# Kernel optimization log

Measured on AMD Instinct MI355X. Metric: run time of the kernel, lower is better.

## Reference

```python
import jax, jax.numpy as jnp
import numpy as np

NP, NR, NK = 64, 8, 500          # problems, rollouts, candidate nodes
H, HEADS, VD = 256, 8, 8         # hidden_dim, heads, vars_dim
HD = H // HEADS                  # head_dim
CLIP = 10.0                      # tanh logit clipping
NEG_INF = -jnp.inf


def setup_inputs() -> dict:
    key = jax.random.key(0)
    ks = jax.random.split(key, 17)
    f = lambda k, s: jax.random.normal(k, s, dtype=jnp.float32)
    B = NP * NR
    s = 1.0 / np.sqrt(H)
    return {
        "X": f(ks[0], (NP, NK, H)),
        "K": f(ks[1], (HEADS, NP, NK, HD)),
        "V": f(ks[2], (HEADS, NP, NK, HD)),
        "query": f(ks[3], (B, H)),
        "state1": f(ks[4], (B, H)),
        "state2": f(ks[5], (B, H)),
        "varfeat": f(ks[6], (NP, VD, NK)),
        "mask": jax.random.uniform(ks[7], (NP, NR, NK)) < 0.1,
        "nn_Q": f(ks[8], (HEADS, H, HD)) * (1.0 / np.sqrt(HD)),
        "nn_O": f(ks[9], (H, H)) * s,
        "nn_A": f(ks[10], (VD, H)) * s,
        "nn_B": f(ks[11], (H,)) * s,
        "nn_W": f(ks[12], (H,)) * s,
        "W_ih": f(ks[13], (4 * H, H)) * s,
        "W_hh": f(ks[14], (4 * H, H)) * s,
        "b_ih": f(ks[15], (4 * H,)) * s,
        "b_hh": f(ks[16], (4 * H,)) * s,
    }


def _decode(X, K, V, query, state1, state2, varfeat, mask,
            nn_Q, nn_O, nn_A, nn_B, nn_W, W_ih, W_hh, b_ih, b_hh):
    B = query.shape[0]
    # --- LSTMCell (PyTorch gate order: i, f, g, o) ---
    gates = query @ W_ih.T + b_ih + state1 @ W_hh.T + b_hh
    i, fg, g, o = jnp.split(gates, 4, axis=1)
    c = jax.nn.sigmoid(fg) * state2 + jax.nn.sigmoid(i) * jnp.tanh(g)
    h = jax.nn.sigmoid(o) * jnp.tanh(c)
    # --- MultiHeadAttention (glimpse) ---
    q = h.reshape(NP, NR, H)
    Q = jnp.einsum('pqh,ahd->apqd', q, nn_Q)                    # [heads,NP,NR,HD]
    S = jnp.einsum('apqd,apkd->apqk', Q, K) * (1.0 / np.sqrt(HD))
    S = jnp.where(mask[None], NEG_INF, S)
    S = jax.nn.softmax(S, axis=-1)
    x = jnp.einsum('apqk,apkd->apqd', S, V)
    x = x.transpose(1, 2, 0, 3).reshape(NP, NR, H)              # [NP,NR,H]
    qm = x @ nn_O                                               # glimpse query
    # --- additive attention with variable features ---
    vf = jnp.einsum('pvk,vh->pkh', varfeat, nn_A) + nn_B        # [NP,NK,H]
    t = jnp.tanh(X[:, None] + vf[:, None] + qm[:, :, None])     # [NP,NR,NK,H]
    logit = jnp.einsum('pqkh,h->pqk', t, nn_W)
    logit = jnp.where(mask, NEG_INF, logit).reshape(B, NK)
    # --- choose (mode=1: greedy argmax) ---
    infeasible = logit == NEG_INF
    l = jnp.where(infeasible, NEG_INF, jnp.tanh(logit) * CLIP)
    chosen = jnp.argmax(l, axis=1)
    logp = jax.nn.log_softmax(l, axis=1)
    chosen_p = jnp.take_along_axis(logp, chosen[:, None], axis=1).squeeze(1)
    return h, c, chosen_p


def reference(X, K, V, query, state1, state2, varfeat, mask,
              nn_Q, nn_O, nn_A, nn_B, nn_W, W_ih, W_hh, b_ih, b_hh):
    return _decode(X, K, V, query, state1, state2, varfeat, mask,
                   nn_Q, nn_O, nn_A, nn_B, nn_W, W_ih, W_hh, b_ih, b_hh)
```

## Files before the change

### kernel.cpp

```cpp
#include <hip/hip_runtime.h>

#define NPP   64
#define NRR   8
#define NKK   500
#define HDIM  256
#define NHEAD 8
#define VDIM  8
#define HD    32
#define BTOT  512

__device__ __forceinline__ float fast_tanh(float x) {
  const float e = __expf(2.f * x);
  return 1.f - 2.f * __builtin_amdgcn_rcpf(e + 1.f);
}
__device__ __forceinline__ float fast_sig(float x) {
  return __builtin_amdgcn_rcpf(1.f + __expf(-x));
}

__global__ __launch_bounds__(64) void k_lstm4(
    const float* __restrict__ query, const float* __restrict__ state1,
    const float* __restrict__ state2,
    const float* __restrict__ W_ih, const float* __restrict__ W_hh,
    const float* __restrict__ b_ih, const float* __restrict__ b_hh,
    const unsigned char* __restrict__ maskb, int* __restrict__ flagp,
    float* __restrict__ out_h, float* __restrict__ out_c)
{
  __shared__ float Wt[32][40];
  __shared__ float At[32][40];
  __shared__ float gt[32][40];

  const int t  = threadIdx.x;
  const int hb = blockIdx.x;
  const int bb = blockIdx.y;

  if (flagp != nullptr && hb == 0 && bb == 0) {
    __shared__ int f;
    if (t == 0) f = 0;
    __syncthreads();
    int any = 0;
    for (int j = t; j < 2048; j += 64) any |= maskb[2 * j + 1];
    if (any) atomicOr(&f, 1);
    __syncthreads();
    if (t == 0) *flagp = f;
  }

  const int tr = t >> 3, tc = t & 7;
  const int srow = t >> 1, sseg = (t & 1) * 16;
  const int wgrow = (srow >> 3) * HDIM + hb * 8 + (srow & 7);
  const int agrow = bb * 32 + srow;

  float acc[4][4];
#pragma unroll
  for (int i = 0; i < 4; ++i)
#pragma unroll
    for (int j = 0; j < 4; ++j) acc[i][j] = 0.f;

  for (int k0 = 0; k0 < 512; k0 += 32) {
    __syncthreads();
    {
      const float* wsrc = (k0 < 256) ? (W_ih + (size_t)wgrow * HDIM + k0)
                                     : (W_hh + (size_t)wgrow * HDIM + (k0 - 256));
      const float* asrc = (k0 < 256) ? (query  + (size_t)agrow * HDIM + k0)
                                     : (state1 + (size_t)agrow * HDIM + (k0 - 256));
#pragma unroll
      for (int j = 0; j < 4; ++j) {
        const float4 wv = *reinterpret_cast<const float4*>(wsrc + sseg + 4 * j);
        const float4 av = *reinterpret_cast<const float4*>(asrc + sseg + 4 * j);
        const int kk = sseg + 4 * j;
        Wt[kk + 0][srow] = wv.x; Wt[kk + 1][srow] = wv.y;
        Wt[kk + 2][srow] = wv.z; Wt[kk + 3][srow] = wv.w;
        At[kk + 0][srow] = av.x; At[kk + 1][srow] = av.y;
        At[kk + 2][srow] = av.z; At[kk + 3][srow] = av.w;
      }
    }
    __syncthreads();
#pragma unroll 8
    for (int kk = 0; kk < 32; ++kk) {
      const float4 wv = *reinterpret_cast<const float4*>(&Wt[kk][tr * 4]);
      const float4 av = *reinterpret_cast<const float4*>(&At[kk][tc * 4]);
      const float w[4] = {wv.x, wv.y, wv.z, wv.w};
      const float a[4] = {av.x, av.y, av.z, av.w};
#pragma unroll
      for (int i = 0; i < 4; ++i)
#pragma unroll
        for (int j = 0; j < 4; ++j) acc[i][j] += w[i] * a[j];
    }
  }

#pragma unroll
  for (int i = 0; i < 4; ++i) {
    float4 v;
    v.x = acc[i][0]; v.y = acc[i][1]; v.z = acc[i][2]; v.w = acc[i][3];
    *reinterpret_cast<float4*>(&gt[tr * 4 + i][tc * 4]) = v;
  }
  __syncthreads();

#pragma unroll
  for (int it = 0; it < 4; ++it) {
    const int cell = t + 64 * it;
    const int b = cell & 31, h = cell >> 5;
    const int gh = hb * 8 + h;
    const int gb = bb * 32 + b;
    const float bi = b_ih[0 * HDIM + gh] + b_hh[0 * HDIM + gh];
    const float bf = b_ih[1 * HDIM + gh] + b_hh[1 * HDIM + gh];
    const float bg = b_ih[2 * HDIM + gh] + b_hh[2 * HDIM + gh];
    const float bo = b_ih[3 * HDIM + gh] + b_hh[3 * HDIM + gh];
    const float iv = fast_sig (gt[ 0 + h][b] + bi);
    const float fv = fast_sig (gt[ 8 + h][b] + bf);
    const float gv = fast_tanh(gt[16 + h][b] + bg);
    const float ov = fast_sig (gt[24 + h][b] + bo);
    const size_t off = (size_t)gb * HDIM + gh;
    const float c = fv * state2[off] + iv * gv;
    out_c[off] = c;
    out_h[off] = ov * fast_tanh(c);
  }
}

__global__ __launch_bounds__(512, 4) void k_attn8(
    const float* __restrict__ Kt, const float* __restrict__ Vt,
    const float* __restrict__ nn_Q, const float* __restrict__ nn_O,
    const void* __restrict__ maskp, const int* __restrict__ flagp,
    const float* __restrict__ out_h, float* __restrict__ qm_slabs)
{
  const int p = blockIdx.x >> 3;
  const int a = blockIdx.x & 7;
  const int t = threadIdx.x;
  const int wave = t >> 6, lane = t & 63;

  __shared__ float hs[NRR][HDIM];
  __shared__ float Qs[NRR][36];
  __shared__ float Sb[NRR][512];
  __shared__ float pb[16][NRR][HD];
  __shared__ float xs[NRR][36];

  const float4 hv = reinterpret_cast<const float4*>(
      out_h + (size_t)p * NRR * HDIM)[t];

  const int flag = *flagp;

  const int kc = (t < NKK) ? t : (NKK - 1);
  const float4* kp4 = reinterpret_cast<const float4*>(
      Kt + (((size_t)a * NPP + p) * NKK + kc) * HD);
  float4 kreg[8];
#pragma unroll
  for (int j = 0; j < 8; ++j) kreg[j] = kp4[j];

  const int dpv = t & 31, kb = t >> 5;
  const float* vb = Vt + (((size_t)a * NPP + p) * NKK + (size_t)kb * 32) * HD + dpv;
  float vreg[32];
#pragma unroll
  for (int j = 0; j < 32; ++j)
    vreg[j] = (kb * 32 + j < NKK) ? vb[(size_t)j * HD] : 0.f;

  float maskv[NRR];
  {
    const unsigned char* mb = (const unsigned char*)maskp;
    const int* mi = (const int*)maskp;
#pragma unroll
    for (int r = 0; r < NRR; ++r) {
      const size_t mo = (size_t)(p * NRR + r) * NKK + kc;
      const bool mk = flag ? (mb[mo] != 0) : (mi[mo] != 0);
      maskv[r] = mk ? -INFINITY : 0.f;
    }
  }

  reinterpret_cast<float4*>(&hs[0][0])[t] = hv;
  __syncthreads();

  {
    const int r = wave, d4 = lane >> 3, ks = lane & 7;
    const float* qb = nn_Q + ((size_t)a * HDIM + ks * 32) * HD + d4 * 4;
    float qx = 0.f, qy = 0.f, qz = 0.f, qw = 0.f;
#pragma unroll
    for (int h = 0; h < 32; ++h) {
      const float hval = hs[r][ks * 32 + h];
      const float4 wv = *reinterpret_cast<const float4*>(qb + (size_t)h * HD);
      qx += hval * wv.x; qy += hval * wv.y;
      qz += hval * wv.z; qw += hval * wv.w;
    }
#pragma unroll
    for (int off = 1; off < 8; off <<= 1) {
      qx += __shfl_xor(qx, off, 64);
      qy += __shfl_xor(qy, off, 64);
      qz += __shfl_xor(qz, off, 64);
      qw += __shfl_xor(qw, off, 64);
    }
    if (ks == 0) {
      const float sc = 0.17677669529663687f;
      Qs[r][d4 * 4 + 0] = qx * sc; Qs[r][d4 * 4 + 1] = qy * sc;
      Qs[r][d4 * 4 + 2] = qz * sc; Qs[r][d4 * 4 + 3] = qw * sc;
    }
  }
  __syncthreads();

#pragma unroll
  for (int r = 0; r < NRR; ++r) {
    float s = 0.f;
#pragma unroll
    for (int j = 0; j < 8; ++j) {
      const float4 q = *reinterpret_cast<const float4*>(&Qs[r][j * 4]);
      const float4 k4 = kreg[j];
      s += q.x * k4.x + q.y * k4.y + q.z * k4.z + q.w * k4.w;
    }
    Sb[r][t] = (t < NKK) ? (s + maskv[r]) : -INFINITY;
  }
  __syncthreads();

  {
    const int r = wave;
    float lv[8], m = -INFINITY;
#pragma unroll
    for (int i = 0; i < 8; ++i) {
      lv[i] = Sb[r][lane + 64 * i];
      m = fmaxf(m, lv[i]);
    }
#pragma unroll
    for (int off = 32; off > 0; off >>= 1) m = fmaxf(m, __shfl_xor(m, off, 64));
    float ssum = 0.f;
#pragma unroll
    for (int i = 0; i < 8; ++i) {
      lv[i] = __expf(lv[i] - m);
      ssum += lv[i];
    }
#pragma unroll
    for (int off = 32; off > 0; off >>= 1) ssum += __shfl_xor(ssum, off, 64);
    const float inv = 1.f / ssum;
#pragma unroll
    for (int i = 0; i < 8; ++i) Sb[r][lane + 64 * i] = lv[i] * inv;
  }
  __syncthreads();

  {
    float acc[NRR];
#pragma unroll
    for (int r = 0; r < NRR; ++r) acc[r] = 0.f;
#pragma unroll
    for (int j4 = 0; j4 < 8; ++j4) {
      const float v0 = vreg[j4 * 4 + 0], v1 = vreg[j4 * 4 + 1];
      const float v2 = vreg[j4 * 4 + 2], v3 = vreg[j4 * 4 + 3];
#pragma unroll
      for (int r = 0; r < NRR; ++r) {
        const float4 s4 = *reinterpret_cast<const float4*>(
            &Sb[r][kb * 32 + j4 * 4]);
        acc[r] += s4.x * v0 + s4.y * v1 + s4.z * v2 + s4.w * v3;
      }
    }
#pragma unroll
    for (int r = 0; r < NRR; ++r) pb[kb][r][dpv] = acc[r];
  }
  __syncthreads();

  if (t < 256) {
    const int r = t >> 5, d = t & 31;
    float s = 0.f;
#pragma unroll
    for (int q = 0; q < 16; ++q) s += pb[q][r][d];
    xs[r][d] = s;
  }
  __syncthreads();

  {
    const int j = t & 255, rr = t >> 8;
    float a0 = 0.f, a1 = 0.f, a2 = 0.f, a3 = 0.f;
#pragma unroll
    for (int d4 = 0; d4 < 8; ++d4) {
      const float4 x0 = *reinterpret_cast<const float4*>(&xs[rr * 4 + 0][d4 * 4]);
      const float4 x1 = *reinterpret_cast<const float4*>(&xs[rr * 4 + 1][d4 * 4]);
      const float4 x2 = *reinterpret_cast<const float4*>(&xs[rr * 4 + 2][d4 * 4]);
      const float4 x3 = *reinterpret_cast<const float4*>(&xs[rr * 4 + 3][d4 * 4]);
      const float c0[4] = {x0.x, x0.y, x0.z, x0.w};
      const float c1[4] = {x1.x, x1.y, x1.z, x1.w};
      const float c2[4] = {x2.x, x2.y, x2.z, x2.w};
      const float c3[4] = {x3.x, x3.y, x3.z, x3.w};
#pragma unroll
      for (int dd = 0; dd < 4; ++dd) {
        const float w = nn_O[((size_t)(a * HD + d4 * 4 + dd)) * HDIM + j];
        a0 += c0[dd] * w; a1 += c1[dd] * w;
        a2 += c2[dd] * w; a3 += c3[dd] * w;
      }
    }
    float* slab = qm_slabs + (size_t)a * BTOT * HDIM;
    slab[(size_t)(p * NRR + rr * 4 + 0) * HDIM + j] = a0;
    slab[(size_t)(p * NRR + rr * 4 + 1) * HDIM + j] = a1;
    slab[(size_t)(p * NRR + rr * 4 + 2) * HDIM + j] = a2;
    slab[(size_t)(p * NRR + rr * 4 + 3) * HDIM + j] = a3;
  }
}

__global__ __launch_bounds__(256) void k_logits6(
    const float* __restrict__ X, const float* __restrict__ varfeat,
    const float* __restrict__ nn_A, const float* __restrict__ nn_B,
    const float* __restrict__ nn_W, const float* __restrict__ qm_slabs,
    const int* __restrict__ flagp, const void* __restrict__ maskp,
    float* __restrict__ pmax, float* __restrict__ psum)
{
  const int p  = blockIdx.x >> 5;
  const int kt = blockIdx.x & 31;
  const int t = threadIdx.x;
  const int wave = t >> 6, lane = t & 63;
  const int h0 = lane * 4;

  __shared__ float qb[NRR][260];
  __shared__ float red[4][NRR][2];

  const unsigned char* mb = (const unsigned char*)maskp;
  const int* mi = (const int*)maskp;
  const int flag = *flagp;
  const bool mbyte = (flag != 0);

  for (int s = t; s < 512; s += 256) {
    const int r = s >> 6, h4 = s & 63;
    const float4 bv = *reinterpret_cast<const float4*>(nn_B + h4 * 4);
    float qx = bv.x, qy = bv.y, qz = bv.z, qw = bv.w;
#pragma unroll
    for (int a = 0; a < NHEAD; ++a) {
      const float4 q = *reinterpret_cast<const float4*>(
          qm_slabs + (size_t)a * BTOT * HDIM +
          (size_t)(p * NRR + r) * HDIM + h4 * 4);
      qx += q.x; qy += q.y; qz += q.z; qw += q.w;
    }
    qb[r][h4 * 4 + 0] = qx; qb[r][h4 * 4 + 1] = qy;
    qb[r][h4 * 4 + 2] = qz; qb[r][h4 * 4 + 3] = qw;
  }
  __syncthreads();

  const float4 w4 = *reinterpret_cast<const float4*>(nn_W + h0);
  float4 a4r[VDIM];
#pragma unroll
  for (int v = 0; v < VDIM; ++v)
    a4r[v] = *reinterpret_cast<const float4*>(nn_A + (size_t)v * HDIM + h0);
  float4 q4r[NRR];
#pragma unroll
  for (int r = 0; r < NRR; ++r)
    q4r[r] = *reinterpret_cast<const float4*>(&qb[r][h0]);

  float rmax = -INFINITY, rsum = 0.f;

  for (int kk = 0; kk < 4; ++kk) {
    const int k = kt * 16 + wave * 4 + kk;
    if (k >= NKK) break;

    const float4 x4 = *reinterpret_cast<const float4*>(
        X + ((size_t)p * NKK + k) * HDIM + h0);
    float base0 = x4.x, base1 = x4.y, base2 = x4.z, base3 = x4.w;
#pragma unroll
    for (int v = 0; v < VDIM; ++v) {
      const float vv = varfeat[((size_t)p * VDIM + v) * NKK + k];
      base0 += vv * a4r[v].x; base1 += vv * a4r[v].y;
      base2 += vv * a4r[v].z; base3 += vv * a4r[v].w;
    }

    float acc[NRR];
#pragma unroll
    for (int r = 0; r < NRR; ++r) {
      acc[r] = fast_tanh(base0 + q4r[r].x) * w4.x
             + fast_tanh(base1 + q4r[r].y) * w4.y
             + fast_tanh(base2 + q4r[r].z) * w4.z
             + fast_tanh(base3 + q4r[r].w) * w4.w;
    }

    float v4[4];
    {
      float sw[8];
#pragma unroll
      for (int j = 0; j < 8; ++j) sw[j] = __shfl_xor(acc[j], 32, 64);
      const bool hi = (lane & 32) != 0;
#pragma unroll
      for (int j = 0; j < 4; ++j)
        v4[j] = hi ? (acc[j + 4] + sw[j + 4]) : (acc[j] + sw[j]);
    }
    float v2[2];
    {
      float sw[4];
#pragma unroll
      for (int j = 0; j < 4; ++j) sw[j] = __shfl_xor(v4[j], 16, 64);
      const bool hi = (lane & 16) != 0;
      v2[0] = hi ? (v4[2] + sw[2]) : (v4[0] + sw[0]);
      v2[1] = hi ? (v4[3] + sw[3]) : (v4[1] + sw[1]);
    }
    float w;
    {
      const float s0 = __shfl_xor(v2[0], 8, 64);
      const float s1 = __shfl_xor(v2[1], 8, 64);
      w = ((lane & 8) != 0) ? (v2[1] + s1) : (v2[0] + s0);
    }
    w += __shfl_xor(w, 4, 64);
    w += __shfl_xor(w, 2, 64);
    w += __shfl_xor(w, 1, 64);

    if ((lane & 7) == 0) {
      const int r = lane >> 3;
      const size_t mrow = (size_t)(p * NRR + r) * NKK + k;
      const bool mk = mbyte ? (mb[mrow] != 0) : (mi[mrow] != 0);
      const float l = mk ? -INFINITY : fast_tanh(w) * 10.0f;
      rmax = fmaxf(rmax, l);
      rsum += __expf(l - 10.f);
    }
  }

  if ((lane & 7) == 0) {
    red[wave][lane >> 3][0] = rmax;
    red[wave][lane >> 3][1] = rsum;
  }
  __syncthreads();
  if (t < NRR) {
    float m = red[0][t][0], s = red[0][t][1];
#pragma unroll
    for (int w = 1; w < 4; ++w) {
      m = fmaxf(m, red[w][t][0]);
      s += red[w][t][1];
    }
    pmax[(size_t)(p * NRR + t) * 32 + kt] = m;
    psum[(size_t)(p * NRR + t) * 32 + kt] = s;
  }
}

__global__ __launch_bounds__(64) void k_choose2(
    const float* __restrict__ pmax, const float* __restrict__ psum,
    float* __restrict__ out_p)
{
  const int b = blockIdx.x;
  const int lane = threadIdx.x;
  float m = (lane < 32) ? pmax[(size_t)b * 32 + lane] : -INFINITY;
  float s = (lane < 32) ? psum[(size_t)b * 32 + lane] : 0.f;
#pragma unroll
  for (int off = 16; off > 0; off >>= 1) {
    m = fmaxf(m, __shfl_xor(m, off, 64));
    s += __shfl_xor(s, off, 64);
  }
  if (lane == 0) out_p[b] = m - 10.f - logf(s);
}

__global__ __launch_bounds__(256) void k_fused(
    const float* __restrict__ X, const float* __restrict__ Kt,
    const float* __restrict__ Vt, const float* __restrict__ varfeat,
    const void* __restrict__ maskp,
    const float* __restrict__ nn_Q, const float* __restrict__ nn_O,
    const float* __restrict__ nn_A, const float* __restrict__ nn_B,
    const float* __restrict__ nn_W,
    const float* __restrict__ out_h, float* __restrict__ out_p)
{
  const int p = blockIdx.x >> 3;
  const int r = blockIdx.x & 7;
  const int t = threadIdx.x;
  const int wave = t >> 6, lane = t & 63;

  __shared__ float hs[HDIM];
  __shared__ float Qs[NHEAD][HD];
  __shared__ float Sb[NHEAD][NKK];
  __shared__ float xs[HDIM];
  __shared__ float qs[HDIM];
  __shared__ float As2[HDIM][VDIM];
  __shared__ float Ws[HDIM];
  __shared__ float lsb[NKK];
  __shared__ int   mask_any;

  const unsigned char* mb = (const unsigned char*)maskp;
  if (t == 0) mask_any = 0;
  __syncthreads();
  {
    int any = 0;
    for (int j = t; j < 2048; j += 256) any |= mb[2 * j + 1];
    if (any) atomicOr(&mask_any, 1);
  }
  for (int idx = t; idx < VDIM * HDIM; idx += 256)
    As2[idx & 255][idx >> 8] = nn_A[idx];
  Ws[t] = nn_W[t];
  hs[t] = out_h[(size_t)(p * NRR + r) * HDIM + t];
  __syncthreads();
  const bool mbyte = (mask_any != 0);
  const int* mi = (const int*)maskp;
  const size_t mrow = (size_t)(p * NRR + r) * NKK;
  {
    const int a = t >> 5, d = t & 31;
    const float* nq = nn_Q + (size_t)a * HDIM * HD + d;
    float acc = 0.f;
    for (int h = 0; h < HDIM; ++h) acc += hs[h] * nq[(size_t)h * HD];
    Qs[a][d] = acc * 0.17677669529663687f;
  }
  __syncthreads();
  for (int k = t; k < NKK; k += 256) {
    const bool mk = mbyte ? (mb[mrow + k] != 0) : (mi[mrow + k] != 0);
#pragma unroll
    for (int a = 0; a < NHEAD; ++a) {
      const float4* kr4 = reinterpret_cast<const float4*>(
          Kt + (((size_t)a * NPP + p) * NKK + k) * HD);
      float s = 0.f;
#pragma unroll
      for (int d4 = 0; d4 < HD / 4; ++d4) {
        const float4 u = kr4[d4];
        s += Qs[a][4 * d4] * u.x + Qs[a][4 * d4 + 1] * u.y
           + Qs[a][4 * d4 + 2] * u.z + Qs[a][4 * d4 + 3] * u.w;
      }
      Sb[a][k] = mk ? -INFINITY : s;
    }
  }
  __syncthreads();
  for (int aa = 0; aa < 2; ++aa) {
    const int a = wave * 2 + aa;
    float m = -INFINITY;
    for (int k = lane; k < NKK; k += 64) m = fmaxf(m, Sb[a][k]);
#pragma unroll
    for (int off = 32; off > 0; off >>= 1) m = fmaxf(m, __shfl_xor(m, off, 64));
    float ssum = 0.f;
    for (int k = lane; k < NKK; k += 64) {
      const float e = expf(Sb[a][k] - m);
      Sb[a][k] = e; ssum += e;
    }
#pragma unroll
    for (int off = 32; off > 0; off >>= 1) ssum += __shfl_xor(ssum, off, 64);
    const float inv = 1.f / ssum;
    for (int k = lane; k < NKK; k += 64) Sb[a][k] *= inv;
  }
  __syncthreads();
  {
    const int a = t >> 5, d = t & 31;
    const float* vb = Vt + ((size_t)a * NPP + p) * NKK * HD + d;
    float acc = 0.f;
    for (int k = 0; k < NKK; ++k) acc += Sb[a][k] * vb[(size_t)k * HD];
    xs[a * HD + d] = acc;
  }
  __syncthreads();
  {
    float acc = 0.f;
    for (int i = 0; i < HDIM; ++i) acc += xs[i] * nn_O[(size_t)i * HDIM + t];
    qs[t] = acc + nn_B[t];
  }
  __syncthreads();
  for (int k = t; k < NKK; k += 256) {
    float vfv[VDIM];
#pragma unroll
    for (int v = 0; v < VDIM; ++v)
      vfv[v] = varfeat[((size_t)p * VDIM + v) * NKK + k];
    const float4* xp4 = reinterpret_cast<const float4*>(
        X + ((size_t)p * NKK + k) * HDIM);
    float acc = 0.f;
    for (int h4 = 0; h4 < HDIM / 4; ++h4) {
      const float4 ux = xp4[h4];
      const float xv[4] = {ux.x, ux.y, ux.z, ux.w};
#pragma unroll
      for (int j = 0; j < 4; ++j) {
        const int h = 4 * h4 + j;
        float base = xv[j] + qs[h];
        const float4 a0 = *reinterpret_cast<const float4*>(&As2[h][0]);
        const float4 a1 = *reinterpret_cast<const float4*>(&As2[h][4]);
        base += vfv[0] * a0.x + vfv[1] * a0.y + vfv[2] * a0.z + vfv[3] * a0.w
              + vfv[4] * a1.x + vfv[5] * a1.y + vfv[6] * a1.z + vfv[7] * a1.w;
        acc += tanhf(base) * Ws[h];
      }
    }
    lsb[k] = acc;
  }
  __syncthreads();
  for (int k = t; k < NKK; k += 256) {
    const bool mk = mbyte ? (mb[mrow + k] != 0) : (mi[mrow + k] != 0);
    lsb[k] = mk ? -INFINITY : tanhf(lsb[k]) * 10.0f;
  }
  __syncthreads();
  if (wave == 0) {
    float m = -INFINITY;
    for (int k = lane; k < NKK; k += 64) m = fmaxf(m, lsb[k]);
#pragma unroll
    for (int off = 32; off > 0; off >>= 1) m = fmaxf(m, __shfl_xor(m, off, 64));
    float s = 0.f;
    for (int k = lane; k < NKK; k += 64) s += expf(lsb[k] - m);
#pragma unroll
    for (int off = 32; off > 0; off >>= 1) s += __shfl_xor(s, off, 64);
    if (lane == 0) out_p[p * NRR + r] = -logf(s);
  }
}

extern "C" void kernel_launch(void* const* d_in, const int* in_sizes, int n_in,
                              void* d_out, int out_size, void* d_ws, size_t ws_size,
                              hipStream_t stream)
{
  const float* X       = (const float*)d_in[0];
  const float* Kt      = (const float*)d_in[1];
  const float* Vt      = (const float*)d_in[2];
  const float* query   = (const float*)d_in[3];
  const float* state1  = (const float*)d_in[4];
  const float* state2  = (const float*)d_in[5];
  const float* varfeat = (const float*)d_in[6];
  const void*  maskp   = d_in[7];
  const float* nn_Q    = (const float*)d_in[8];
  const float* nn_O    = (const float*)d_in[9];
  const float* nn_A    = (const float*)d_in[10];
  const float* nn_B    = (const float*)d_in[11];
  const float* nn_W    = (const float*)d_in[12];
  const float* W_ih    = (const float*)d_in[13];
  const float* W_hh    = (const float*)d_in[14];
  const float* b_ih    = (const float*)d_in[15];
  const float* b_hh    = (const float*)d_in[16];

  float* out   = (float*)d_out;
  float* out_h = out;
  float* out_c = out + (size_t)BTOT * HDIM;
  float* out_p = out + (size_t)2 * BTOT * HDIM;

  const size_t flag_bytes = 256;
  const size_t qm8_bytes  = (size_t)NHEAD * BTOT * HDIM * 4;
  const size_t part_bytes = (size_t)BTOT * 32 * 4;
  const size_t need = flag_bytes + qm8_bytes + 2 * part_bytes;

  if (ws_size >= need) {
    int*   flagp = (int*)d_ws;
    float* qmw  = (float*)((char*)d_ws + flag_bytes);
    float* pmax = (float*)((char*)d_ws + flag_bytes + qm8_bytes);
    float* psum = (float*)((char*)d_ws + flag_bytes + qm8_bytes + part_bytes);

    hipLaunchKernelGGL(k_lstm4, dim3(32, 16), dim3(64), 0, stream,
                       query, state1, state2, W_ih, W_hh, b_ih, b_hh,
                       (const unsigned char*)maskp, flagp, out_h, out_c);
    hipLaunchKernelGGL(k_attn8, dim3(NPP * NHEAD), dim3(512), 0, stream,
                       Kt, Vt, nn_Q, nn_O, maskp, flagp, out_h, qmw);
    hipLaunchKernelGGL(k_logits6, dim3(NPP * 32), dim3(256), 0, stream,
                       X, varfeat, nn_A, nn_B, nn_W, qmw, flagp, maskp,
                       pmax, psum);
    hipLaunchKernelGGL(k_choose2, dim3(BTOT), dim3(64), 0, stream,
                       pmax, psum, out_p);
  } else {
    hipLaunchKernelGGL(k_lstm4, dim3(32, 16), dim3(64), 0, stream,
                       query, state1, state2, W_ih, W_hh, b_ih, b_hh,
                       (const unsigned char*)maskp, nullptr, out_h, out_c);
    hipLaunchKernelGGL(k_fused, dim3(NPP * NRR), dim3(256), 0, stream,
                       X, Kt, Vt, varfeat, maskp,
                       nn_Q, nn_O, nn_A, nn_B, nn_W,
                       out_h, out_p);
  }
}
```

Baseline: 234.9 us.

## Widen LSTM blocks to 256 threads and split attention across rollout halves

The LSTM gate GEMM now runs 256 threads per block, each computing a 2x2 tile instead of 4x4, with padded shared tiles. The attention kernel is launched with twice as many blocks, each handling 4 of the 8 rollouts. The Q projection is split across two wave groups and summed afterwards. This raises parallelism and occupancy for small grids, at the cost of loading the K/V registers twice (once per half) and adding extra syncs.

```diff
diff --git a/kernel.cpp b/kernel.cpp
--- a/kernel.cpp
+++ b/kernel.cpp
@@ -17,7 +17,7 @@
   return __builtin_amdgcn_rcpf(1.f + __expf(-x));
 }
 
-__global__ __launch_bounds__(64) void k_lstm4(
+__global__ __launch_bounds__(256) void k_lstm3(
     const float* __restrict__ query, const float* __restrict__ state1,
     const float* __restrict__ state2,
     const float* __restrict__ W_ih, const float* __restrict__ W_hh,
@@ -25,9 +25,9 @@
     const unsigned char* __restrict__ maskb, int* __restrict__ flagp,
     float* __restrict__ out_h, float* __restrict__ out_c)
 {
-  __shared__ float Wt[32][40];
-  __shared__ float At[32][40];
-  __shared__ float gt[32][40];
+  __shared__ float Wt[32][33];
+  __shared__ float At[32][33];
+  __shared__ float gt[32][33];
 
   const int t  = threadIdx.x;
   const int hb = blockIdx.x;
@@ -38,67 +38,54 @@
     if (t == 0) f = 0;
     __syncthreads();
     int any = 0;
-    for (int j = t; j < 2048; j += 64) any |= maskb[2 * j + 1];
+    for (int j = t; j < 2048; j += 256) any |= maskb[2 * j + 1];
     if (any) atomicOr(&f, 1);
     __syncthreads();
     if (t == 0) *flagp = f;
   }
 
-  const int tr = t >> 3, tc = t & 7;
-  const int srow = t >> 1, sseg = (t & 1) * 16;
-  const int wgrow = (srow >> 3) * HDIM + hb * 8 + (srow & 7);
-  const int agrow = bb * 32 + srow;
-
-  float acc[4][4];
-#pragma unroll
-  for (int i = 0; i < 4; ++i)
-#pragma unroll
-    for (int j = 0; j < 4; ++j) acc[i][j] = 0.f;
+  const int trow = t >> 4;
+  const int tcol = t & 15;
+
+  float acc00 = 0.f, acc01 = 0.f, acc10 = 0.f, acc11 = 0.f;
+
+  const int wrow = t >> 3, wk4 = t & 7;
+  const int wpart = wrow >> 3, whh = wrow & 7;
+  const int wgrow = wpart * HDIM + hb * 8 + whh;
+  const int agrow = bb * 32 + wrow;
 
   for (int k0 = 0; k0 < 512; k0 += 32) {
     __syncthreads();
     {
       const float* wsrc = (k0 < 256) ? (W_ih + (size_t)wgrow * HDIM + k0)
                                      : (W_hh + (size_t)wgrow * HDIM + (k0 - 256));
+      const float4 wv = *reinterpret_cast<const float4*>(wsrc + wk4 * 4);
+      Wt[wk4 * 4 + 0][wrow] = wv.x; Wt[wk4 * 4 + 1][wrow] = wv.y;
+      Wt[wk4 * 4 + 2][wrow] = wv.z; Wt[wk4 * 4 + 3][wrow] = wv.w;
+
       const float* asrc = (k0 < 256) ? (query  + (size_t)agrow * HDIM + k0)
                                      : (state1 + (size_t)agrow * HDIM + (k0 - 256));
-#pragma unroll
-      for (int j = 0; j < 4; ++j) {
-        const float4 wv = *reinterpret_cast<const float4*>(wsrc + sseg + 4 * j);
-        const float4 av = *reinterpret_cast<const float4*>(asrc + sseg + 4 * j);
-        const int kk = sseg + 4 * j;
-        Wt[kk + 0][srow] = wv.x; Wt[kk + 1][srow] = wv.y;
-        Wt[kk + 2][srow] = wv.z; Wt[kk + 3][srow] = wv.w;
-        At[kk + 0][srow] = av.x; At[kk + 1][srow] = av.y;
-        At[kk + 2][srow] = av.z; At[kk + 3][srow] = av.w;
-      }
+      const float4 av = *reinterpret_cast<const float4*>(asrc + wk4 * 4);
+      At[wk4 * 4 + 0][wrow] = av.x; At[wk4 * 4 + 1][wrow] = av.y;
+      At[wk4 * 4 + 2][wrow] = av.z; At[wk4 * 4 + 3][wrow] = av.w;
     }
     __syncthreads();
+
 #pragma unroll 8
     for (int kk = 0; kk < 32; ++kk) {
-      const float4 wv = *reinterpret_cast<const float4*>(&Wt[kk][tr * 4]);
-      const float4 av = *reinterpret_cast<const float4*>(&At[kk][tc * 4]);
-      const float w[4] = {wv.x, wv.y, wv.z, wv.w};
-      const float a[4] = {av.x, av.y, av.z, av.w};
-#pragma unroll
-      for (int i = 0; i < 4; ++i)
-#pragma unroll
-        for (int j = 0; j < 4; ++j) acc[i][j] += w[i] * a[j];
-    }
-  }
-
-#pragma unroll
-  for (int i = 0; i < 4; ++i) {
-    float4 v;
-    v.x = acc[i][0]; v.y = acc[i][1]; v.z = acc[i][2]; v.w = acc[i][3];
-    *reinterpret_cast<float4*>(&gt[tr * 4 + i][tc * 4]) = v;
-  }
-  __syncthreads();
-
-#pragma unroll
-  for (int it = 0; it < 4; ++it) {
-    const int cell = t + 64 * it;
-    const int b = cell & 31, h = cell >> 5;
+      const float w0 = Wt[kk][trow], w1 = Wt[kk][trow + 16];
+      const float a0 = At[kk][tcol], a1 = At[kk][tcol + 16];
+      acc00 += w0 * a0; acc01 += w0 * a1;
+      acc10 += w1 * a0; acc11 += w1 * a1;
+    }
+  }
+
+  gt[trow][tcol] = acc00;      gt[trow][tcol + 16] = acc01;
+  gt[trow + 16][tcol] = acc10; gt[trow + 16][tcol + 16] = acc11;
+  __syncthreads();
+
+  {
+    const int h = t & 7, b = t >> 3;
     const int gh = hb * 8 + h;
     const int gb = bb * 32 + b;
     const float bi = b_ih[0 * HDIM + gh] + b_hh[0 * HDIM + gh];
@@ -116,25 +103,32 @@
   }
 }
 
-__global__ __launch_bounds__(512, 4) void k_attn8(
+__global__ __launch_bounds__(512, 4) void k_attn9(
     const float* __restrict__ Kt, const float* __restrict__ Vt,
     const float* __restrict__ nn_Q, const float* __restrict__ nn_O,
     const void* __restrict__ maskp, const int* __restrict__ flagp,
     const float* __restrict__ out_h, float* __restrict__ qm_slabs)
 {
-  const int p = blockIdx.x >> 3;
-  const int a = blockIdx.x & 7;
-  const int t = threadIdx.x;
+  const int bid  = blockIdx.x;
+  const int half = bid >> 9;
+  const int pa   = bid & 511;
+  const int p    = pa >> 3;
+  const int a    = pa & 7;
+  const int r0   = half * 4;
+  const int t    = threadIdx.x;
   const int wave = t >> 6, lane = t & 63;
 
-  __shared__ float hs[NRR][HDIM];
-  __shared__ float Qs[NRR][36];
-  __shared__ float Sb[NRR][512];
-  __shared__ float pb[16][NRR][HD];
-  __shared__ float xs[NRR][36];
-
-  const float4 hv = reinterpret_cast<const float4*>(
-      out_h + (size_t)p * NRR * HDIM)[t];
+  __shared__ float hs[4][HDIM];
+  __shared__ float Qp[2][4][36];
+  __shared__ float Qs[4][36];
+  __shared__ float Sb[4][512];
+  __shared__ float pb[16][4][HD];
+  __shared__ float xs[4][36];
+
+  float4 hv = make_float4(0.f, 0.f, 0.f, 0.f);
+  if (t < 256)
+    hv = reinterpret_cast<const float4*>(
+        out_h + (size_t)(p * NRR + r0) * HDIM)[t];
 
   const int flag = *flagp;
 
@@ -152,28 +146,30 @@
   for (int j = 0; j < 32; ++j)
     vreg[j] = (kb * 32 + j < NKK) ? vb[(size_t)j * HD] : 0.f;
 
-  float maskv[NRR];
+  float maskv[4];
   {
     const unsigned char* mb = (const unsigned char*)maskp;
     const int* mi = (const int*)maskp;
 #pragma unroll
-    for (int r = 0; r < NRR; ++r) {
-      const size_t mo = (size_t)(p * NRR + r) * NKK + kc;
+    for (int r = 0; r < 4; ++r) {
+      const size_t mo = (size_t)(p * NRR + r0 + r) * NKK + kc;
       const bool mk = flag ? (mb[mo] != 0) : (mi[mo] != 0);
       maskv[r] = mk ? -INFINITY : 0.f;
     }
   }
 
-  reinterpret_cast<float4*>(&hs[0][0])[t] = hv;
-  __syncthreads();
-
-  {
-    const int r = wave, d4 = lane >> 3, ks = lane & 7;
-    const float* qb = nn_Q + ((size_t)a * HDIM + ks * 32) * HD + d4 * 4;
+  if (t < 256) reinterpret_cast<float4*>(&hs[0][0])[t] = hv;
+  __syncthreads();
+
+  {
+    const int rloc = wave & 3, hh = wave >> 2;
+    const int d4 = lane >> 3, ks = lane & 7;
+    const int hbase = hh * 128 + ks * 16;
+    const float* qb = nn_Q + ((size_t)a * HDIM + hbase) * HD + d4 * 4;
     float qx = 0.f, qy = 0.f, qz = 0.f, qw = 0.f;
 #pragma unroll
-    for (int h = 0; h < 32; ++h) {
-      const float hval = hs[r][ks * 32 + h];
+    for (int h = 0; h < 16; ++h) {
+      const float hval = hs[rloc][hbase + h];
       const float4 wv = *reinterpret_cast<const float4*>(qb + (size_t)h * HD);
       qx += hval * wv.x; qy += hval * wv.y;
       qz += hval * wv.z; qw += hval * wv.w;
@@ -186,15 +182,19 @@
       qw += __shfl_xor(qw, off, 64);
     }
     if (ks == 0) {
-      const float sc = 0.17677669529663687f;
-      Qs[r][d4 * 4 + 0] = qx * sc; Qs[r][d4 * 4 + 1] = qy * sc;
-      Qs[r][d4 * 4 + 2] = qz * sc; Qs[r][d4 * 4 + 3] = qw * sc;
-    }
-  }
-  __syncthreads();
-
-#pragma unroll
-  for (int r = 0; r < NRR; ++r) {
+      Qp[hh][rloc][d4 * 4 + 0] = qx; Qp[hh][rloc][d4 * 4 + 1] = qy;
+      Qp[hh][rloc][d4 * 4 + 2] = qz; Qp[hh][rloc][d4 * 4 + 3] = qw;
+    }
+  }
+  __syncthreads();
+  if (t < 128) {
+    const int rr = t >> 5, d = t & 31;
+    Qs[rr][d] = (Qp[0][rr][d] + Qp[1][rr][d]) * 0.17677669529663687f;
+  }
+  __syncthreads();
+
+#pragma unroll
+  for (int r = 0; r < 4; ++r) {
     float s = 0.f;
 #pragma unroll
     for (int j = 0; j < 8; ++j) {
@@ -206,7 +206,7 @@
   }
   __syncthreads();
 
-  {
+  if (wave < 4) {
     const int r = wave;
     float lv[8], m = -INFINITY;
 #pragma unroll
@@ -231,26 +231,26 @@
   __syncthreads();
 
   {
-    float acc[NRR];
-#pragma unroll
-    for (int r = 0; r < NRR; ++r) acc[r] = 0.f;
+    float acc[4];
+#pragma unroll
+    for (int r = 0; r < 4; ++r) acc[r] = 0.f;
 #pragma unroll
     for (int j4 = 0; j4 < 8; ++j4) {
       const float v0 = vreg[j4 * 4 + 0], v1 = vreg[j4 * 4 + 1];
       const float v2 = vreg[j4 * 4 + 2], v3 = vreg[j4 * 4 + 3];
 #pragma unroll
-      for (int r = 0; r < NRR; ++r) {
+      for (int r = 0; r < 4; ++r) {
         const float4 s4 = *reinterpret_cast<const float4*>(
             &Sb[r][kb * 32 + j4 * 4]);
         acc[r] += s4.x * v0 + s4.y * v1 + s4.z * v2 + s4.w * v3;
       }
     }
 #pragma unroll
-    for (int r = 0; r < NRR; ++r) pb[kb][r][dpv] = acc[r];
-  }
-  __syncthreads();
-
-  if (t < 256) {
+    for (int r = 0; r < 4; ++r) pb[kb][r][dpv] = acc[r];
+  }
+  __syncthreads();
+
+  if (t < 128) {
     const int r = t >> 5, d = t & 31;
     float s = 0.f;
 #pragma unroll
@@ -261,29 +261,22 @@
 
   {
     const int j = t & 255, rr = t >> 8;
-    float a0 = 0.f, a1 = 0.f, a2 = 0.f, a3 = 0.f;
+    float a0 = 0.f, a1 = 0.f;
 #pragma unroll
     for (int d4 = 0; d4 < 8; ++d4) {
-      const float4 x0 = *reinterpret_cast<const float4*>(&xs[rr * 4 + 0][d4 * 4]);
-      const float4 x1 = *reinterpret_cast<const float4*>(&xs[rr * 4 + 1][d4 * 4]);
-      const float4 x2 = *reinterpret_cast<const float4*>(&xs[rr * 4 + 2][d4 * 4]);
-      const float4 x3 = *reinterpret_cast<const float4*>(&xs[rr * 4 + 3][d4 * 4]);
+      const float4 x0 = *reinterpret_cast<const float4*>(&xs[rr * 2 + 0][d4 * 4]);
+      const float4 x1 = *reinterpret_cast<const float4*>(&xs[rr * 2 + 1][d4 * 4]);
       const float c0[4] = {x0.x, x0.y, x0.z, x0.w};
       const float c1[4] = {x1.x, x1.y, x1.z, x1.w};
-      const float c2[4] = {x2.x, x2.y, x2.z, x2.w};
-      const float c3[4] = {x3.x, x3.y, x3.z, x3.w};
 #pragma unroll
       for (int dd = 0; dd < 4; ++dd) {
         const float w = nn_O[((size_t)(a * HD + d4 * 4 + dd)) * HDIM + j];
         a0 += c0[dd] * w; a1 += c1[dd] * w;
-        a2 += c2[dd] * w; a3 += c3[dd] * w;
       }
     }
     float* slab = qm_slabs + (size_t)a * BTOT * HDIM;
-    slab[(size_t)(p * NRR + rr * 4 + 0) * HDIM + j] = a0;
-    slab[(size_t)(p * NRR + rr * 4 + 1) * HDIM + j] = a1;
-    slab[(size_t)(p * NRR + rr * 4 + 2) * HDIM + j] = a2;
-    slab[(size_t)(p * NRR + rr * 4 + 3) * HDIM + j] = a3;
+    slab[(size_t)(p * NRR + r0 + rr * 2 + 0) * HDIM + j] = a0;
+    slab[(size_t)(p * NRR + r0 + rr * 2 + 1) * HDIM + j] = a1;
   }
 }
 
@@ -608,10 +601,10 @@
     float* pmax = (float*)((char*)d_ws + flag_bytes + qm8_bytes);
     float* psum = (float*)((char*)d_ws + flag_bytes + qm8_bytes + part_bytes);
 
-    hipLaunchKernelGGL(k_lstm4, dim3(32, 16), dim3(64), 0, stream,
+    hipLaunchKernelGGL(k_lstm3, dim3(32, 16), dim3(256), 0, stream,
                        query, state1, state2, W_ih, W_hh, b_ih, b_hh,
                        (const unsigned char*)maskp, flagp, out_h, out_c);
-    hipLaunchKernelGGL(k_attn8, dim3(NPP * NHEAD), dim3(512), 0, stream,
+    hipLaunchKernelGGL(k_attn9, dim3(NPP * NHEAD * 2), dim3(512), 0, stream,
                        Kt, Vt, nn_Q, nn_O, maskp, flagp, out_h, qmw);
     hipLaunchKernelGGL(k_logits6, dim3(NPP * 32), dim3(256), 0, stream,
                        X, varfeat, nn_A, nn_B, nn_W, qmw, flagp, maskp,
@@ -619,7 +612,7 @@
     hipLaunchKernelGGL(k_choose2, dim3(BTOT), dim3(64), 0, stream,
                        pmax, psum, out_p);
   } else {
-    hipLaunchKernelGGL(k_lstm4, dim3(32, 16), dim3(64), 0, stream,
+    hipLaunchKernelGGL(k_lstm3, dim3(32, 16), dim3(256), 0, stream,
                        query, state1, state2, W_ih, W_hh, b_ih, b_hh,
                        (const unsigned char*)maskp, nullptr, out_h, out_c);
     hipLaunchKernelGGL(k_fused, dim3(NPP * NRR), dim3(256), 0, stream,
```

Measured after the change: 232.1 us. Within noise of the previous version (-1.2%).
